# Performance work log

Hardware: AMD Instinct MI355X
Metric: run time of the kernel (lower is better)

## Reference

```python
import jax, jax.numpy as jnp
import numpy as np

N, E, D = 100000, 1600000, 128      # nodes, edges, in_channels = MLP out_dim
L = 3                               # num GIN layers
OC = D + L * D                      # concat width = 512
CH, CHID = 4, 256                   # num ChannelMLPs, their hidden dim


def setup_inputs() -> dict:
    key = jax.random.key(0)
    ks = jax.random.split(key, 10)
    s = lambda fan_in: 1.0 / np.sqrt(fan_in)
    x = jax.random.normal(ks[0], (N, D), dtype=jnp.float32)
    edge_index = jax.random.randint(ks[1], (2, E), 0, N, dtype=jnp.int32)
    # conv MLPs: per layer 3 linear layers (in->hid, hid->hid, hid->out), all 128x128
    convW = jax.random.normal(ks[2], (L, 3, D, D), dtype=jnp.float32) * s(D)
    convB = jnp.zeros((L, 3, D), dtype=jnp.float32)
    # channel MLPs: 512 -> 256 -> 256 -> 1, ReLU after every layer (output_activation='relu')
    chanW1 = jax.random.normal(ks[3], (CH, OC, CHID), dtype=jnp.float32) * s(OC)
    chanB1 = jnp.zeros((CH, CHID), dtype=jnp.float32)
    chanW2 = jax.random.normal(ks[4], (CH, CHID, CHID), dtype=jnp.float32) * s(CHID)
    chanB2 = jnp.zeros((CH, CHID), dtype=jnp.float32)
    chanW3 = jax.random.normal(ks[5], (CH, CHID, 1), dtype=jnp.float32) * s(CHID)
    chanB3 = jnp.zeros((CH, 1), dtype=jnp.float32)
    return {"x": x, "edge_index": edge_index, "convW": convW, "convB": convB,
            "chanW1": chanW1, "chanB1": chanB1, "chanW2": chanW2, "chanB2": chanB2,
            "chanW3": chanW3, "chanB3": chanB3}


def reference(x, edge_index, convW, convB, chanW1, chanB1, chanW2, chanB2, chanW3, chanB3):
    src, dst = edge_index[0], edge_index[1]
    n = x.shape[0]
    feats = [x]                      # skip_first_features=False -> keep input
    h = x
    for l in range(L):
        # GINConv, eps=0: mlp((1+eps)*h + sum_{j in N(i)} h_j)
        agg = jax.ops.segment_sum(h[src], dst, num_segments=n)  # scatter-add at targets
        h = h + agg
        for k in range(3):           # MLP: Lin+ReLU x3 (2 hidden + relu output activation)
            h = jax.nn.relu(h @ convW[l, k] + convB[l, k])
        feats.append(h)
    xcat = jnp.concatenate(feats, axis=1)                       # [N, 512]
    # channel MLPs vectorized over the channel axis c
    h1 = jax.nn.relu(jnp.einsum('nd,cdh->cnh', xcat, chanW1) + chanB1[:, None, :])
    h2 = jax.nn.relu(jnp.einsum('cnh,chk->cnk', h1, chanW2) + chanB2[:, None, :])
    h3 = jax.nn.relu(jnp.einsum('cnh,cho->cno', h2, chanW3) + chanB3[:, None, :])
    return jnp.transpose(h3[..., 0])                            # [N, num_ChannelMLPs]
```

## Files before the change

### kernel.cpp

```cpp
#include <hip/hip_runtime.h>
#include <hip/hip_bf16.h>

#define D 128
#define NLAYER 3
#define NCH 4

typedef __attribute__((ext_vector_type(8))) short short8;
typedef __attribute__((ext_vector_type(4))) float f32x4;

__device__ __forceinline__ ushort f2bf(float f) {
    unsigned int u = __builtin_bit_cast(unsigned int, f);
    u += 0x7fffu + ((u >> 16) & 1u);
    return (ushort)(u >> 16);
}
__device__ __forceinline__ float bflo(unsigned int u) {
    return __builtin_bit_cast(float, u << 16);
}
__device__ __forceinline__ float bfhi(unsigned int u) {
    return __builtin_bit_cast(float, u & 0xffff0000u);
}

#define FILL_CHUNK 4096
__global__ __launch_bounds__(256) void hist_part_kernel(
    const int* __restrict__ dst, int* __restrict__ deg,
    int E, int nPer, int N)
{
    int cls = blockIdx.x & 7;
    int base = (blockIdx.x >> 3) * FILL_CHUNK;
    int lo = cls * nPer;
    int hi = lo + nPer; if (hi > N) hi = N;
    int end = base + FILL_CHUNK; if (end > E) end = E;
    for (int e = base + threadIdx.x; e < end; e += 256) {
        int d = dst[e];
        if (d >= lo && d < hi) atomicAdd(&deg[d], 1);
    }
}

__global__ __launch_bounds__(256) void blocksum_kernel(
    const int* __restrict__ deg, int* __restrict__ bsum, int n)
{
    int i = blockIdx.x * 256 + threadIdx.x;
    int v = (i < n) ? deg[i] : 0;
#pragma unroll
    for (int o = 1; o < 64; o <<= 1) v += __shfl_xor(v, o);
    __shared__ int s[4];
    if ((threadIdx.x & 63) == 0) s[threadIdx.x >> 6] = v;
    __syncthreads();
    if (threadIdx.x == 0) bsum[blockIdx.x] = s[0] + s[1] + s[2] + s[3];
}

__global__ __launch_bounds__(512) void scanblk_kernel(
    const int* __restrict__ bsum, int* __restrict__ boff, int nb,
    int* __restrict__ offs, int n, int E)
{
    __shared__ int sh[512];
    int t = threadIdx.x;
    sh[t] = (t < nb) ? bsum[t] : 0;
    __syncthreads();
    for (int d = 1; d < 512; d <<= 1) {
        int v = (t >= d) ? sh[t - d] : 0;
        __syncthreads();
        sh[t] += v;
        __syncthreads();
    }
    if (t < nb) boff[t] = (t == 0) ? 0 : sh[t - 1];
    if (t == 0) offs[n] = E;
}

__global__ __launch_bounds__(256) void blockscan_kernel(
    const int* __restrict__ deg, const int* __restrict__ boff,
    int* __restrict__ offs, int* __restrict__ cursor, int n)
{
    __shared__ int sh[256];
    int t = threadIdx.x;
    int i = blockIdx.x * 256 + t;
    int v = (i < n) ? deg[i] : 0;
    sh[t] = v;
    __syncthreads();
    for (int d = 1; d < 256; d <<= 1) {
        int u = (t >= d) ? sh[t - d] : 0;
        __syncthreads();
        sh[t] += u;
        __syncthreads();
    }
    if (i < n) {
        int ex = boff[blockIdx.x] + sh[t] - v;
        offs[i] = ex; cursor[i] = ex;
    }
}

__global__ __launch_bounds__(256) void fill_part_kernel(
    const int* __restrict__ src, const int* __restrict__ dst,
    int* __restrict__ cursor, int* __restrict__ csr,
    int E, int nPer, int N)
{
    int cls = blockIdx.x & 7;
    int base = (blockIdx.x >> 3) * FILL_CHUNK;
    int lo = cls * nPer;
    int hi = lo + nPer; if (hi > N) hi = N;
    int end = base + FILL_CHUNK; if (end > E) end = E;
    for (int e = base + threadIdx.x; e < end; e += 256) {
        int d = dst[e];
        int s = src[e];
        if (d >= lo && d < hi) {
            int p = atomicAdd(&cursor[d], 1);
            csr[p] = s;
        }
    }
}

__global__ __launch_bounds__(256) void cvtx_kernel(
    const float* __restrict__ x, ushort* __restrict__ xb, int total8)
{
    int i = blockIdx.x * 256 + threadIdx.x;
    if (i >= total8) return;
    const float* gp = x + (size_t)i * 8;
    float4 v0 = *(const float4*)gp;
    float4 v1 = *(const float4*)(gp + 4);
    short8 pk;
    pk[0] = (short)f2bf(v0.x); pk[1] = (short)f2bf(v0.y);
    pk[2] = (short)f2bf(v0.z); pk[3] = (short)f2bf(v0.w);
    pk[4] = (short)f2bf(v1.x); pk[5] = (short)f2bf(v1.y);
    pk[6] = (short)f2bf(v1.z); pk[7] = (short)f2bf(v1.w);
    *(short8*)(xb + (size_t)i * 8) = pk;
}

__global__ void cvtW_kernel(const float* __restrict__ W, ushort* __restrict__ Wt,
                            int K, int Ncols) {
    __shared__ float tile[32][33];
    int c = blockIdx.z;
    int k0 = blockIdx.x * 32, n0 = blockIdx.y * 32;
    const float* Wc = W + (size_t)c * K * Ncols;
    ushort* Wtc = Wt + (size_t)c * K * Ncols;
    int tx = threadIdx.x & 31, ty = threadIdx.x >> 5;
#pragma unroll
    for (int i = 0; i < 4; ++i) {
        int k = k0 + ty + i * 8;
        tile[ty + i * 8][tx] = Wc[(size_t)k * Ncols + n0 + tx];
    }
    __syncthreads();
#pragma unroll
    for (int i = 0; i < 4; ++i) {
        int n = n0 + ty + i * 8;
        Wtc[(size_t)n * K + k0 + tx] = f2bf(tile[tx][ty + i * 8]);
    }
}

__global__ __launch_bounds__(256) void agg_bf16(
    const ushort* __restrict__ h,
    const int* __restrict__ offs, const int* __restrict__ csr,
    ushort* __restrict__ outb, int n)
{
    int wid = (blockIdx.x * 256 + threadIdx.x) >> 6;
    int lane = threadIdx.x & 63;
    if (wid >= n) return;
    const unsigned int* hb = (const unsigned int*)h;
    unsigned int u = hb[(size_t)wid * 64 + lane];
    float ax = bflo(u), ay = bfhi(u);
    int b = offs[wid], e = offs[wid + 1];
    int j = b;
    for (; j + 4 <= e; j += 4) {
        int s0 = csr[j], s1 = csr[j + 1], s2 = csr[j + 2], s3 = csr[j + 3];
        unsigned int u0 = hb[(size_t)s0 * 64 + lane];
        unsigned int u1 = hb[(size_t)s1 * 64 + lane];
        unsigned int u2 = hb[(size_t)s2 * 64 + lane];
        unsigned int u3 = hb[(size_t)s3 * 64 + lane];
        ax += (bflo(u0) + bflo(u1)) + (bflo(u2) + bflo(u3));
        ay += (bfhi(u0) + bfhi(u1)) + (bfhi(u2) + bfhi(u3));
    }
    for (; j < e; ++j) {
        unsigned int u0 = hb[(size_t)csr[j] * 64 + lane];
        ax += bflo(u0); ay += bfhi(u0);
    }
    unsigned int po = (unsigned int)f2bf(ax) | ((unsigned int)f2bf(ay) << 16);
    ((unsigned int*)outb)[(size_t)wid * 64 + lane] = po;
}

__global__ __launch_bounds__(256) void gin_mlp_mfma(
    const ushort* __restrict__ A,
    const ushort* __restrict__ WtL,
    const float* __restrict__ biasL,
    ushort* __restrict__ Out,
    int nrows)
{
    __shared__ __align__(16) ushort As[128 * 128];
    __shared__ __align__(16) ushort Bs[128 * 128];
    const int t = threadIdx.x;
    const int w = t >> 6, lane = t & 63;
    const int quad = lane >> 4, c15 = lane & 15;
    const int wr = w >> 1, wc = w & 1;
    const int rowbase = blockIdx.x * 128;

#pragma unroll
    for (int i = 0; i < 8; ++i) {
        int lin = (i * 4 + w) * 64 + lane;
        int row = lin >> 4, slot = lin & 15, g = slot ^ (row & 15);
        int grow = rowbase + row;
        if (grow >= nrows) grow = 0;
        const ushort* gp = A + (size_t)grow * 128 + g * 8;
        __builtin_amdgcn_global_load_lds(
            (const __attribute__((address_space(1))) void*)gp,
            (__attribute__((address_space(3))) void*)&As[(i * 4 + w) * 512],
            16, 0, 0);
    }
#pragma unroll
    for (int i = 0; i < 8; ++i) {
        int lin = (i * 4 + w) * 64 + lane;
        int n = lin >> 4, slot = lin & 15, g = slot ^ (n & 15);
        const ushort* gp = WtL + (size_t)n * 128 + g * 8;
        __builtin_amdgcn_global_load_lds(
            (const __attribute__((address_space(1))) void*)gp,
            (__attribute__((address_space(3))) void*)&Bs[(i * 4 + w) * 512],
            16, 0, 0);
    }
    __syncthreads();

    for (int s = 0; s < 3; ++s) {
        f32x4 acc[4][4];
#pragma unroll
        for (int i = 0; i < 4; ++i)
#pragma unroll
            for (int j = 0; j < 4; ++j)
#pragma unroll
                for (int r = 0; r < 4; ++r) acc[i][j][r] = 0.f;

#pragma unroll
        for (int ks = 0; ks < 4; ++ks) {
            short8 af[4], bf[4];
#pragma unroll
            for (int tr = 0; tr < 4; ++tr) {
                int r = wr * 64 + tr * 16 + c15;
                af[tr] = *(const short8*)&As[r * 128 + (((ks * 4 + quad) ^ (r & 15)) * 8)];
            }
#pragma unroll
            for (int tc = 0; tc < 4; ++tc) {
                int n = wc * 64 + tc * 16 + c15;
                bf[tc] = *(const short8*)&Bs[n * 128 + (((ks * 4 + quad) ^ (n & 15)) * 8)];
            }
#pragma unroll
            for (int tr = 0; tr < 4; ++tr)
#pragma unroll
                for (int tc = 0; tc < 4; ++tc)
                    acc[tr][tc] = __builtin_amdgcn_mfma_f32_16x16x32_bf16(
                        af[tr], bf[tc], acc[tr][tc], 0, 0, 0);
        }
        __syncthreads();

        if (s < 2) {
#pragma unroll
            for (int tc = 0; tc < 4; ++tc) {
                int col = wc * 64 + tc * 16 + c15;
                float bv = biasL[s * 128 + col];
#pragma unroll
                for (int tr = 0; tr < 4; ++tr)
#pragma unroll
                    for (int rg = 0; rg < 4; ++rg) {
                        int row = wr * 64 + tr * 16 + quad * 4 + rg;
                        As[row * 128 + (((col >> 3) ^ (row & 15)) * 8) + (col & 7)]
                            = f2bf(fmaxf(acc[tr][tc][rg] + bv, 0.f));
                    }
            }
            const ushort* Wn = WtL + (size_t)(s + 1) * 128 * 128;
#pragma unroll
            for (int i = 0; i < 8; ++i) {
                int lin = (i * 4 + w) * 64 + lane;
                int n = lin >> 4, slot = lin & 15, g = slot ^ (n & 15);
                const ushort* gp = Wn + (size_t)n * 128 + g * 8;
                __builtin_amdgcn_global_load_lds(
                    (const __attribute__((address_space(1))) void*)gp,
                    (__attribute__((address_space(3))) void*)&Bs[(i * 4 + w) * 512],
                    16, 0, 0);
            }
            __syncthreads();
        } else {
#pragma unroll
            for (int tc = 0; tc < 4; ++tc) {
                int col = wc * 64 + tc * 16 + c15;
                float bv = biasL[2 * 128 + col];
#pragma unroll
                for (int tr = 0; tr < 4; ++tr)
#pragma unroll
                    for (int rg = 0; rg < 4; ++rg) {
                        int grow = rowbase + wr * 64 + tr * 16 + quad * 4 + rg;
                        if (grow < nrows)
                            Out[(size_t)grow * 128 + col]
                                = f2bf(fmaxf(acc[tr][tc][rg] + bv, 0.f));
                    }
            }
        }
    }
}

__global__ __launch_bounds__(256, 2) void chan_fused_mfma(
    const ushort* __restrict__ A0, const ushort* __restrict__ A1,
    const ushort* __restrict__ A2, const ushort* __restrict__ A3,
    const ushort* __restrict__ Wt1,
    const float* __restrict__ b1,
    const ushort* __restrict__ Wt2,
    const float* __restrict__ b2,
    const float* __restrict__ w3,
    const float* __restrict__ b3,
    float* __restrict__ out,
    int N, int T, int chunkT)
{
    const int bid = blockIdx.x;
    const int xcd = bid & 7;
    const int idx = bid >> 3;
    const int c = idx & 3;
    const int rt = xcd * chunkT + (idx >> 2);
    if (rt >= T) return;
    const int rowbase = rt * 64;

    __shared__ __align__(16) ushort As[64 * 64];
    __shared__ __align__(16) ushort Bs[256 * 64];
    __shared__ __align__(16) ushort Ts[64 * 256];
    __shared__ float red[64][4];
    const int t = threadIdx.x;
    const int w = t >> 6, lane = t & 63;
    const int quad = lane >> 4, c15 = lane & 15;
    const ushort* Asrc[4] = {A0, A1, A2, A3};
    const ushort* W1c = Wt1 + (size_t)c * 256 * 512;
    const ushort* W2c = Wt2 + (size_t)c * 256 * 256;

    f32x4 acc[4][4];
#pragma unroll
    for (int i = 0; i < 4; ++i)
#pragma unroll
        for (int j = 0; j < 4; ++j)
#pragma unroll
            for (int r = 0; r < 4; ++r) acc[i][j][r] = 0.f;

    for (int kc = 0; kc < 512; kc += 64) {
        const ushort* Ab = Asrc[kc >> 7];
        const int within = kc & 127;
#pragma unroll
        for (int i = 0; i < 2; ++i) {
            int lin = (i * 4 + w) * 64 + lane;
            int row = lin >> 3, slot = lin & 7, g = slot ^ (row & 7);
            int grow = rowbase + row;
            if (grow >= N) grow = 0;
            const ushort* gp = Ab + (size_t)grow * 128 + within + g * 8;
            __builtin_amdgcn_global_load_lds(
                (const __attribute__((address_space(1))) void*)gp,
                (__attribute__((address_space(3))) void*)&As[(i * 4 + w) * 512],
                16, 0, 0);
        }
#pragma unroll
        for (int i = 0; i < 8; ++i) {
            int lin = (i * 4 + w) * 64 + lane;
            int n = lin >> 3, slot = lin & 7, g = slot ^ (n & 7);
            const ushort* gp = W1c + (size_t)n * 512 + kc + g * 8;
            __builtin_amdgcn_global_load_lds(
                (const __attribute__((address_space(1))) void*)gp,
                (__attribute__((address_space(3))) void*)&Bs[(i * 4 + w) * 512],
                16, 0, 0);
        }
        __syncthreads();
#pragma unroll
        for (int ks = 0; ks < 2; ++ks) {
            const int K8 = ks * 4;
            short8 af[4], bf[4];
#pragma unroll
            for (int tr = 0; tr < 4; ++tr) {
                int r = tr * 16 + c15;
                af[tr] = *(const short8*)&As[r * 64 + (((K8 + quad) ^ (r & 7)) * 8)];
            }
#pragma unroll
            for (int tc = 0; tc < 4; ++tc) {
                int n = w * 64 + tc * 16 + c15;
                bf[tc] = *(const short8*)&Bs[n * 64 + (((K8 + quad) ^ (n & 7)) * 8)];
            }
#pragma unroll
            for (int tr = 0; tr < 4; ++tr)
#pragma unroll
                for (int tc = 0; tc < 4; ++tc)
                    acc[tr][tc] = __builtin_amdgcn_mfma_f32_16x16x32_bf16(
                        af[tr], bf[tc], acc[tr][tc], 0, 0, 0);
        }
        __syncthreads();
    }

#pragma unroll
    for (int tc = 0; tc < 4; ++tc) {
        int col = w * 64 + tc * 16 + c15;
        float bv = b1[c * 256 + col];
#pragma unroll
        for (int tr = 0; tr < 4; ++tr)
#pragma unroll
            for (int rg = 0; rg < 4; ++rg) {
                int row = tr * 16 + quad * 4 + rg;
                Ts[row * 256 + (((col >> 3) ^ (row & 31)) * 8) + (col & 7)]
                    = f2bf(fmaxf(acc[tr][tc][rg] + bv, 0.f));
            }
    }
    __syncthreads();

#pragma unroll
    for (int i = 0; i < 4; ++i)
#pragma unroll
        for (int j = 0; j < 4; ++j)
#pragma unroll
            for (int r = 0; r < 4; ++r) acc[i][j][r] = 0.f;

    for (int kc = 0; kc < 256; kc += 64) {
#pragma unroll
        for (int i = 0; i < 8; ++i) {
            int lin = (i * 4 + w) * 64 + lane;
            int n = lin >> 3, slot = lin & 7, g = slot ^ (n & 7);
            const ushort* gp = W2c + (size_t)n * 256 + kc + g * 8;
            __builtin_amdgcn_global_load_lds(
                (const __attribute__((address_space(1))) void*)gp,
                (__attribute__((address_space(3))) void*)&Bs[(i * 4 + w) * 512],
                16, 0, 0);
        }
        __syncthreads();
#pragma unroll
        for (int ks = 0; ks < 2; ++ks) {
            short8 af[4], bf[4];
            const int g0 = (kc >> 3) + ks * 4 + quad;
#pragma unroll
            for (int tr = 0; tr < 4; ++tr) {
                int r = tr * 16 + c15;
                af[tr] = *(const short8*)&Ts[r * 256 + ((g0 ^ (r & 31)) * 8)];
            }
#pragma unroll
            for (int tc = 0; tc < 4; ++tc) {
                int n = w * 64 + tc * 16 + c15;
                bf[tc] = *(const short8*)&Bs[n * 64 + ((((ks * 4) + quad) ^ (n & 7)) * 8)];
            }
#pragma unroll
            for (int tr = 0; tr < 4; ++tr)
#pragma unroll
                for (int tc = 0; tc < 4; ++tc)
                    acc[tr][tc] = __builtin_amdgcn_mfma_f32_16x16x32_bf16(
                        af[tr], bf[tc], acc[tr][tc], 0, 0, 0);
        }
        __syncthreads();
    }

    float b2v[4], w3v[4];
#pragma unroll
    for (int tc = 0; tc < 4; ++tc) {
        int col = w * 64 + tc * 16 + c15;
        b2v[tc] = b2[c * 256 + col];
        w3v[tc] = w3[c * 256 + col];
    }
#pragma unroll
    for (int tr = 0; tr < 4; ++tr)
#pragma unroll
        for (int rg = 0; rg < 4; ++rg) {
            float p = 0.f;
#pragma unroll
            for (int tc = 0; tc < 4; ++tc)
                p += fmaxf(acc[tr][tc][rg] + b2v[tc], 0.f) * w3v[tc];
            p += __shfl_xor(p, 1);
            p += __shfl_xor(p, 2);
            p += __shfl_xor(p, 4);
            p += __shfl_xor(p, 8);
            if (c15 == 0) red[tr * 16 + quad * 4 + rg][w] = p;
        }
    __syncthreads();
    if (t < 64) {
        int grow = rowbase + t;
        if (grow < N) {
            float s = red[t][0] + red[t][1] + red[t][2] + red[t][3] + b3[c];
            out[(size_t)grow * NCH + c] = fmaxf(s, 0.f);
        }
    }
}

extern "C" void kernel_launch(void* const* d_in, const int* in_sizes, int n_in,
                              void* d_out, int out_size, void* d_ws, size_t ws_size,
                              hipStream_t stream) {
    const float* x        = (const float*)d_in[0];
    const int*   eidx     = (const int*)d_in[1];
    const float* convW    = (const float*)d_in[2];
    const float* convB    = (const float*)d_in[3];
    const float* chanW1   = (const float*)d_in[4];
    const float* chanB1   = (const float*)d_in[5];
    const float* chanW2   = (const float*)d_in[6];
    const float* chanB2   = (const float*)d_in[7];
    const float* chanW3   = (const float*)d_in[8];
    const float* chanB3   = (const float*)d_in[9];
    float* out = (float*)d_out;

    const int N = in_sizes[0] / D;
    const int E = in_sizes[1] / 2;
    const int* srcp = eidx;
    const int* dstp = eidx + E;
    const int nb = (N + 255) / 256;

    char* w = (char*)d_ws;
    auto take = [&](size_t bytes) {
        char* p = w;
        w += (bytes + 255) & ~(size_t)255;
        return p;
    };
    ushort* xb     = (ushort*)take((size_t)N * D * 2);
    ushort* h0     = (ushort*)take((size_t)N * D * 2);
    ushort* h1     = (ushort*)take((size_t)N * D * 2);
    ushort* h2     = (ushort*)take((size_t)N * D * 2);
    int*    deg    = (int*)take((size_t)N * 4);
    int*    offs   = (int*)take((size_t)(N + 1) * 4);
    int*    cursor = (int*)take((size_t)N * 4);
    int*    bsum   = (int*)take((size_t)nb * 4);
    int*    boff   = (int*)take((size_t)nb * 4);
    ushort* Wt1b   = (ushort*)take((size_t)NCH * 256 * 512 * 2);
    ushort* Wt2b   = (ushort*)take((size_t)NCH * 256 * 256 * 2);
    ushort* WtC    = (ushort*)take((size_t)NLAYER * 3 * D * D * 2);

    size_t used = (size_t)(w - (char*)d_ws);
    if (used > ws_size) return;
    size_t rem = ws_size - used;
    size_t need_gin = (((size_t)E * 4 + 255) & ~(size_t)255) + (size_t)N * D * 2;
    if (rem < need_gin) return;

    int*    csr = (int*)w;
    ushort* a   = (ushort*)(w + (((size_t)E * 4 + 255) & ~(size_t)255));

    hipMemsetAsync(deg, 0, (size_t)N * 4, stream);
    {
        int nchunks = (E + FILL_CHUNK - 1) / FILL_CHUNK;
        int nPer = (N + 7) / 8;
        hist_part_kernel<<<nchunks * 8, 256, 0, stream>>>(dstp, deg, E, nPer, N);
        blocksum_kernel<<<nb, 256, 0, stream>>>(deg, bsum, N);
        scanblk_kernel<<<1, 512, 0, stream>>>(bsum, boff, nb, offs, N, E);
        blockscan_kernel<<<nb, 256, 0, stream>>>(deg, boff, offs, cursor, N);
        fill_part_kernel<<<nchunks * 8, 256, 0, stream>>>(
            srcp, dstp, cursor, csr, E, nPer, N);
    }

    cvtx_kernel<<<(N * 16 + 255) / 256, 256, 0, stream>>>(x, xb, N * 16);
    cvtW_kernel<<<dim3(512 / 32, 256 / 32, NCH), 256, 0, stream>>>(chanW1, Wt1b, 512, 256);
    cvtW_kernel<<<dim3(256 / 32, 256 / 32, NCH), 256, 0, stream>>>(chanW2, Wt2b, 256, 256);
    cvtW_kernel<<<dim3(D / 32, D / 32, NLAYER * 3), 256, 0, stream>>>(convW, WtC, D, D);

    const int rowtiles = (N + 127) / 128;
    const int aggblocks = (N * 64 + 255) / 256;

    ushort* hbuf[NLAYER] = {h0, h1, h2};
    const ushort* prev = xb;
    for (int l = 0; l < NLAYER; ++l) {
        agg_bf16<<<aggblocks, 256, 0, stream>>>(prev, offs, csr, a, N);
        gin_mlp_mfma<<<rowtiles, 256, 0, stream>>>(
            a, WtC + (size_t)l * 3 * D * D, convB + (size_t)l * 3 * D, hbuf[l], N);
        prev = hbuf[l];
    }

    {
        const int T = (N + 63) / 64;
        const int chunkT = (T + 7) / 8;
        const int grid = 8 * chunkT * NCH;
        chan_fused_mfma<<<grid, 256, 0, stream>>>(
            xb, h0, h1, h2,
            Wt1b, chanB1, Wt2b, chanB2, chanW3, chanB3,
            out, N, T, chunkT);
    }
}
```

Before: 860.1 us.

## Fuse neighbor aggregation into GIN MLP kernel, writing sums directly to LDS

Removes the separate aggregation kernel and its intermediate global buffer by having each MLP block gather neighbor features for its 128 rows and write the bf16 sums straight into the swizzled LDS A tile. This saves a full-size global write and read per layer plus a kernel launch. In exchange, the latency-bound gather now runs with far fewer concurrent waves, since each wave walks 32 rows serially under a large-LDS, low-occupancy block.

```diff
diff --git a/kernel.cpp b/kernel.cpp
--- a/kernel.cpp
+++ b/kernel.cpp
@@ -146,42 +146,13 @@
     }
 }
 
-__global__ __launch_bounds__(256) void agg_bf16(
-    const ushort* __restrict__ h,
+__global__ __launch_bounds__(256) void gin_layer_mfma(
+    const ushort* __restrict__ prev,
     const int* __restrict__ offs, const int* __restrict__ csr,
-    ushort* __restrict__ outb, int n)
-{
-    int wid = (blockIdx.x * 256 + threadIdx.x) >> 6;
-    int lane = threadIdx.x & 63;
-    if (wid >= n) return;
-    const unsigned int* hb = (const unsigned int*)h;
-    unsigned int u = hb[(size_t)wid * 64 + lane];
-    float ax = bflo(u), ay = bfhi(u);
-    int b = offs[wid], e = offs[wid + 1];
-    int j = b;
-    for (; j + 4 <= e; j += 4) {
-        int s0 = csr[j], s1 = csr[j + 1], s2 = csr[j + 2], s3 = csr[j + 3];
-        unsigned int u0 = hb[(size_t)s0 * 64 + lane];
-        unsigned int u1 = hb[(size_t)s1 * 64 + lane];
-        unsigned int u2 = hb[(size_t)s2 * 64 + lane];
-        unsigned int u3 = hb[(size_t)s3 * 64 + lane];
-        ax += (bflo(u0) + bflo(u1)) + (bflo(u2) + bflo(u3));
-        ay += (bfhi(u0) + bfhi(u1)) + (bfhi(u2) + bfhi(u3));
-    }
-    for (; j < e; ++j) {
-        unsigned int u0 = hb[(size_t)csr[j] * 64 + lane];
-        ax += bflo(u0); ay += bfhi(u0);
-    }
-    unsigned int po = (unsigned int)f2bf(ax) | ((unsigned int)f2bf(ay) << 16);
-    ((unsigned int*)outb)[(size_t)wid * 64 + lane] = po;
-}
-
-__global__ __launch_bounds__(256) void gin_mlp_mfma(
-    const ushort* __restrict__ A,
     const ushort* __restrict__ WtL,
     const float* __restrict__ biasL,
     ushort* __restrict__ Out,
-    int nrows)
+    int N)
 {
     __shared__ __align__(16) ushort As[128 * 128];
     __shared__ __align__(16) ushort Bs[128 * 128];
@@ -191,18 +162,6 @@
     const int wr = w >> 1, wc = w & 1;
     const int rowbase = blockIdx.x * 128;
 
-#pragma unroll
-    for (int i = 0; i < 8; ++i) {
-        int lin = (i * 4 + w) * 64 + lane;
-        int row = lin >> 4, slot = lin & 15, g = slot ^ (row & 15);
-        int grow = rowbase + row;
-        if (grow >= nrows) grow = 0;
-        const ushort* gp = A + (size_t)grow * 128 + g * 8;
-        __builtin_amdgcn_global_load_lds(
-            (const __attribute__((address_space(1))) void*)gp,
-            (__attribute__((address_space(3))) void*)&As[(i * 4 + w) * 512],
-            16, 0, 0);
-    }
 #pragma unroll
     for (int i = 0; i < 8; ++i) {
         int lin = (i * 4 + w) * 64 + lane;
@@ -213,6 +172,39 @@
             (__attribute__((address_space(3))) void*)&Bs[(i * 4 + w) * 512],
             16, 0, 0);
     }
+
+    {
+        const unsigned int* hb = (const unsigned int*)prev;
+        unsigned int* Asw = (unsigned int*)As;
+        const int gidx = (lane >> 2);
+        const int sub = (lane & 3);
+        for (int rr = 0; rr < 32; ++rr) {
+            int row = w * 32 + rr;
+            int node = rowbase + row;
+            float ax = 0.f, ay = 0.f;
+            if (node < N) {
+                unsigned int u = hb[(size_t)node * 64 + lane];
+                ax = bflo(u); ay = bfhi(u);
+                int b = offs[node], e = offs[node + 1];
+                int j = b;
+                for (; j + 4 <= e; j += 4) {
+                    int s0 = csr[j], s1 = csr[j + 1], s2 = csr[j + 2], s3 = csr[j + 3];
+                    unsigned int u0 = hb[(size_t)s0 * 64 + lane];
+                    unsigned int u1 = hb[(size_t)s1 * 64 + lane];
+                    unsigned int u2 = hb[(size_t)s2 * 64 + lane];
+                    unsigned int u3 = hb[(size_t)s3 * 64 + lane];
+                    ax += (bflo(u0) + bflo(u1)) + (bflo(u2) + bflo(u3));
+                    ay += (bfhi(u0) + bfhi(u1)) + (bfhi(u2) + bfhi(u3));
+                }
+                for (; j < e; ++j) {
+                    unsigned int u0 = hb[(size_t)csr[j] * 64 + lane];
+                    ax += bflo(u0); ay += bfhi(u0);
+                }
+            }
+            unsigned int po = (unsigned int)f2bf(ax) | ((unsigned int)f2bf(ay) << 16);
+            Asw[row * 64 + ((gidx ^ (row & 15)) * 4) + sub] = po;
+        }
+    }
     __syncthreads();
 
     for (int s = 0; s < 3; ++s) {
@@ -282,7 +274,7 @@
 #pragma unroll
                     for (int rg = 0; rg < 4; ++rg) {
                         int grow = rowbase + wr * 64 + tr * 16 + quad * 4 + rg;
-                        if (grow < nrows)
+                        if (grow < N)
                             Out[(size_t)grow * 128 + col]
                                 = f2bf(fmaxf(acc[tr][tc][rg] + bv, 0.f));
                     }
@@ -512,11 +504,9 @@
     size_t used = (size_t)(w - (char*)d_ws);
     if (used > ws_size) return;
     size_t rem = ws_size - used;
-    size_t need_gin = (((size_t)E * 4 + 255) & ~(size_t)255) + (size_t)N * D * 2;
-    if (rem < need_gin) return;
-
-    int*    csr = (int*)w;
-    ushort* a   = (ushort*)(w + (((size_t)E * 4 + 255) & ~(size_t)255));
+    if (rem < (size_t)E * 4) return;
+
+    int* csr = (int*)w;
 
     hipMemsetAsync(deg, 0, (size_t)N * 4, stream);
     {
@@ -536,14 +526,13 @@
     cvtW_kernel<<<dim3(D / 32, D / 32, NLAYER * 3), 256, 0, stream>>>(convW, WtC, D, D);
 
     const int rowtiles = (N + 127) / 128;
-    const int aggblocks = (N * 64 + 255) / 256;
 
     ushort* hbuf[NLAYER] = {h0, h1, h2};
     const ushort* prev = xb;
     for (int l = 0; l < NLAYER; ++l) {
-        agg_bf16<<<aggblocks, 256, 0, stream>>>(prev, offs, csr, a, N);
-        gin_mlp_mfma<<<rowtiles, 256, 0, stream>>>(
-            a, WtC + (size_t)l * 3 * D * D, convB + (size_t)l * 3 * D, hbuf[l], N);
+        gin_layer_mfma<<<rowtiles, 256, 0, stream>>>(
+            prev, offs, csr,
+            WtC + (size_t)l * 3 * D * D, convB + (size_t)l * 3 * D, hbuf[l], N);
         prev = hbuf[l];
     }
 
```

Result: slower. 1.811 ms (+110.6%).

## Process two 64-row tiles per block in channel MLP to reuse W1 tiles

Applied to the files above, without the earlier changes.

The fused channel-MLP kernel now handles 128 rows per block as two 64-row halves. Each W1 K-chunk is loaded into LDS once and used for both halves' first-layer MFMAs, and the grid is halved. This cuts global and LDS traffic for W1 but doubles accumulator registers (two 4x4 f32x4 sets), adds barriers, and halves the number of blocks, which risks spills, lower occupancy and poorer load balance. W2 is still reloaded separately for each half.

```diff
diff --git a/kernel.cpp b/kernel.cpp
--- a/kernel.cpp
+++ b/kernel.cpp
@@ -309,7 +309,8 @@
     const int c = idx & 3;
     const int rt = xcd * chunkT + (idx >> 2);
     if (rt >= T) return;
-    const int rowbase = rt * 64;
+    const int rowbaseA = rt * 128;
+    const int rowbaseB = rowbaseA + 64;
 
     __shared__ __align__(16) ushort As[64 * 64];
     __shared__ __align__(16) ushort Bs[256 * 64];
@@ -322,13 +323,13 @@
     const ushort* W1c = Wt1 + (size_t)c * 256 * 512;
     const ushort* W2c = Wt2 + (size_t)c * 256 * 256;
 
-    f32x4 acc[4][4];
+    f32x4 accA[4][4], accB[4][4];
 #pragma unroll
     for (int i = 0; i < 4; ++i)
 #pragma unroll
         for (int j = 0; j < 4; ++j)
 #pragma unroll
-            for (int r = 0; r < 4; ++r) acc[i][j][r] = 0.f;
+            for (int r = 0; r < 4; ++r) { accA[i][j][r] = 0.f; accB[i][j][r] = 0.f; }
 
     for (int kc = 0; kc < 512; kc += 64) {
         const ushort* Ab = Asrc[kc >> 7];
@@ -337,7 +338,7 @@
         for (int i = 0; i < 2; ++i) {
             int lin = (i * 4 + w) * 64 + lane;
             int row = lin >> 3, slot = lin & 7, g = slot ^ (row & 7);
-            int grow = rowbase + row;
+            int grow = rowbaseA + row;
             if (grow >= N) grow = 0;
             const ushort* gp = Ab + (size_t)grow * 128 + within + g * 8;
             __builtin_amdgcn_global_load_lds(
@@ -374,98 +375,139 @@
             for (int tr = 0; tr < 4; ++tr)
 #pragma unroll
                 for (int tc = 0; tc < 4; ++tc)
-                    acc[tr][tc] = __builtin_amdgcn_mfma_f32_16x16x32_bf16(
-                        af[tr], bf[tc], acc[tr][tc], 0, 0, 0);
-        }
-        __syncthreads();
-    }
-
-#pragma unroll
-    for (int tc = 0; tc < 4; ++tc) {
-        int col = w * 64 + tc * 16 + c15;
-        float bv = b1[c * 256 + col];
-#pragma unroll
-        for (int tr = 0; tr < 4; ++tr)
-#pragma unroll
-            for (int rg = 0; rg < 4; ++rg) {
-                int row = tr * 16 + quad * 4 + rg;
-                Ts[row * 256 + (((col >> 3) ^ (row & 31)) * 8) + (col & 7)]
-                    = f2bf(fmaxf(acc[tr][tc][rg] + bv, 0.f));
-            }
-    }
-    __syncthreads();
-
-#pragma unroll
-    for (int i = 0; i < 4; ++i)
-#pragma unroll
-        for (int j = 0; j < 4; ++j)
-#pragma unroll
-            for (int r = 0; r < 4; ++r) acc[i][j][r] = 0.f;
-
-    for (int kc = 0; kc < 256; kc += 64) {
-#pragma unroll
-        for (int i = 0; i < 8; ++i) {
+                    accA[tr][tc] = __builtin_amdgcn_mfma_f32_16x16x32_bf16(
+                        af[tr], bf[tc], accA[tr][tc], 0, 0, 0);
+        }
+        __syncthreads();
+#pragma unroll
+        for (int i = 0; i < 2; ++i) {
             int lin = (i * 4 + w) * 64 + lane;
-            int n = lin >> 3, slot = lin & 7, g = slot ^ (n & 7);
-            const ushort* gp = W2c + (size_t)n * 256 + kc + g * 8;
+            int row = lin >> 3, slot = lin & 7, g = slot ^ (row & 7);
+            int grow = rowbaseB + row;
+            if (grow >= N) grow = 0;
+            const ushort* gp = Ab + (size_t)grow * 128 + within + g * 8;
             __builtin_amdgcn_global_load_lds(
                 (const __attribute__((address_space(1))) void*)gp,
-                (__attribute__((address_space(3))) void*)&Bs[(i * 4 + w) * 512],
+                (__attribute__((address_space(3))) void*)&As[(i * 4 + w) * 512],
                 16, 0, 0);
         }
         __syncthreads();
 #pragma unroll
         for (int ks = 0; ks < 2; ++ks) {
+            const int K8 = ks * 4;
             short8 af[4], bf[4];
-            const int g0 = (kc >> 3) + ks * 4 + quad;
 #pragma unroll
             for (int tr = 0; tr < 4; ++tr) {
                 int r = tr * 16 + c15;
-                af[tr] = *(const short8*)&Ts[r * 256 + ((g0 ^ (r & 31)) * 8)];
+                af[tr] = *(const short8*)&As[r * 64 + (((K8 + quad) ^ (r & 7)) * 8)];
             }
 #pragma unroll
             for (int tc = 0; tc < 4; ++tc) {
                 int n = w * 64 + tc * 16 + c15;
-                bf[tc] = *(const short8*)&Bs[n * 64 + ((((ks * 4) + quad) ^ (n & 7)) * 8)];
+                bf[tc] = *(const short8*)&Bs[n * 64 + (((K8 + quad) ^ (n & 7)) * 8)];
             }
 #pragma unroll
             for (int tr = 0; tr < 4; ++tr)
 #pragma unroll
                 for (int tc = 0; tc < 4; ++tc)
-                    acc[tr][tc] = __builtin_amdgcn_mfma_f32_16x16x32_bf16(
-                        af[tr], bf[tc], acc[tr][tc], 0, 0, 0);
-        }
-        __syncthreads();
-    }
-
-    float b2v[4], w3v[4];
-#pragma unroll
-    for (int tc = 0; tc < 4; ++tc) {
-        int col = w * 64 + tc * 16 + c15;
-        b2v[tc] = b2[c * 256 + col];
-        w3v[tc] = w3[c * 256 + col];
-    }
-#pragma unroll
-    for (int tr = 0; tr < 4; ++tr)
-#pragma unroll
-        for (int rg = 0; rg < 4; ++rg) {
-            float p = 0.f;
-#pragma unroll
-            for (int tc = 0; tc < 4; ++tc)
-                p += fmaxf(acc[tr][tc][rg] + b2v[tc], 0.f) * w3v[tc];
-            p += __shfl_xor(p, 1);
-            p += __shfl_xor(p, 2);
-            p += __shfl_xor(p, 4);
-            p += __shfl_xor(p, 8);
-            if (c15 == 0) red[tr * 16 + quad * 4 + rg][w] = p;
-        }
-    __syncthreads();
-    if (t < 64) {
-        int grow = rowbase + t;
-        if (grow < N) {
-            float s = red[t][0] + red[t][1] + red[t][2] + red[t][3] + b3[c];
-            out[(size_t)grow * NCH + c] = fmaxf(s, 0.f);
-        }
+                    accB[tr][tc] = __builtin_amdgcn_mfma_f32_16x16x32_bf16(
+                        af[tr], bf[tc], accB[tr][tc], 0, 0, 0);
+        }
+        __syncthreads();
+    }
+
+    for (int half = 0; half < 2; ++half) {
+        const int rowbase = half ? rowbaseB : rowbaseA;
+        f32x4 (*accP)[4] = half ? accB : accA;
+
+#pragma unroll
+        for (int tc = 0; tc < 4; ++tc) {
+            int col = w * 64 + tc * 16 + c15;
+            float bv = b1[c * 256 + col];
+#pragma unroll
+            for (int tr = 0; tr < 4; ++tr)
+#pragma unroll
+                for (int rg = 0; rg < 4; ++rg) {
+                    int row = tr * 16 + quad * 4 + rg;
+                    Ts[row * 256 + (((col >> 3) ^ (row & 31)) * 8) + (col & 7)]
+                        = f2bf(fmaxf(accP[tr][tc][rg] + bv, 0.f));
+                }
+        }
+        __syncthreads();
+
+#pragma unroll
+        for (int i = 0; i < 4; ++i)
+#pragma unroll
+            for (int j = 0; j < 4; ++j)
+#pragma unroll
+                for (int r = 0; r < 4; ++r) accP[i][j][r] = 0.f;
+
+        for (int kc = 0; kc < 256; kc += 64) {
+#pragma unroll
+            for (int i = 0; i < 8; ++i) {
+                int lin = (i * 4 + w) * 64 + lane;
+                int n = lin >> 3, slot = lin & 7, g = slot ^ (n & 7);
+                const ushort* gp = W2c + (size_t)n * 256 + kc + g * 8;
+                __builtin_amdgcn_global_load_lds(
+                    (const __attribute__((address_space(1))) void*)gp,
+                    (__attribute__((address_space(3))) void*)&Bs[(i * 4 + w) * 512],
+                    16, 0, 0);
+            }
+            __syncthreads();
+#pragma unroll
+            for (int ks = 0; ks < 2; ++ks) {
+                short8 af[4], bf[4];
+                const int g0 = (kc >> 3) + ks * 4 + quad;
+#pragma unroll
+                for (int tr = 0; tr < 4; ++tr) {
+                    int r = tr * 16 + c15;
+                    af[tr] = *(const short8*)&Ts[r * 256 + ((g0 ^ (r & 31)) * 8)];
+                }
+#pragma unroll
+                for (int tc = 0; tc < 4; ++tc) {
+                    int n = w * 64 + tc * 16 + c15;
+                    bf[tc] = *(const short8*)&Bs[n * 64 + ((((ks * 4) + quad) ^ (n & 7)) * 8)];
+                }
+#pragma unroll
+                for (int tr = 0; tr < 4; ++tr)
+#pragma unroll
+                    for (int tc = 0; tc < 4; ++tc)
+                        accP[tr][tc] = __builtin_amdgcn_mfma_f32_16x16x32_bf16(
+                            af[tr], bf[tc], accP[tr][tc], 0, 0, 0);
+            }
+            __syncthreads();
+        }
+
+        float b2v[4], w3v[4];
+#pragma unroll
+        for (int tc = 0; tc < 4; ++tc) {
+            int col = w * 64 + tc * 16 + c15;
+            b2v[tc] = b2[c * 256 + col];
+            w3v[tc] = w3[c * 256 + col];
+        }
+#pragma unroll
+        for (int tr = 0; tr < 4; ++tr)
+#pragma unroll
+            for (int rg = 0; rg < 4; ++rg) {
+                float p = 0.f;
+#pragma unroll
+                for (int tc = 0; tc < 4; ++tc)
+                    p += fmaxf(accP[tr][tc][rg] + b2v[tc], 0.f) * w3v[tc];
+                p += __shfl_xor(p, 1);
+                p += __shfl_xor(p, 2);
+                p += __shfl_xor(p, 4);
+                p += __shfl_xor(p, 8);
+                if (c15 == 0) red[tr * 16 + quad * 4 + rg][w] = p;
+            }
+        __syncthreads();
+        if (t < 64) {
+            int grow = rowbase + t;
+            if (grow < N) {
+                float s = red[t][0] + red[t][1] + red[t][2] + red[t][3] + b3[c];
+                out[(size_t)grow * NCH + c] = fmaxf(s, 0.f);
+            }
+        }
+        __syncthreads();
     }
 }
 
@@ -548,7 +590,7 @@
     }
 
     {
-        const int T = (N + 63) / 64;
+        const int T = (N + 127) / 128;
         const int chunkT = (T + 7) / 8;
         const int grid = 8 * chunkT * NCH;
         chan_fused_mfma<<<grid, 256, 0, stream>>>(
```

Measured after the change: 1.320 ms. +53.5%, slower.
